# Kernel optimization log

Hardware: AMD Instinct MI355X
Metric: run time of the kernel (lower is better)

## Reference

```python
import jax, jax.numpy as jnp
import numpy as np

CODEBOOK_SIZE = 1024
EMBEDDING_DIM = 256
COMMITMENT_COST = 0.25


def setup_inputs() -> dict:
    key = jax.random.key(0)
    k1, k2 = jax.random.split(key)
    x = jax.random.normal(k1, (32, EMBEDDING_DIM, 32, 32), dtype=jnp.float32)
    # embedding initialized uniform(-1/K, 1/K) like the torch module
    embedding = jax.random.uniform(
        k2, (CODEBOOK_SIZE, EMBEDDING_DIM), dtype=jnp.float32,
        minval=-1.0 / CODEBOOK_SIZE, maxval=1.0 / CODEBOOK_SIZE)
    return {"x": x, "embedding": embedding}


def reference(x, embedding):
    # x: [B, C, H, W] -> inputs: [B, H, W, C]
    inputs = jnp.transpose(x, (0, 2, 3, 1))
    input_shape = inputs.shape
    flat = inputs.reshape(-1, EMBEDDING_DIM)  # [N, D]
    # squared L2 distances to codebook: [N, K]
    distances = (jnp.sum(flat ** 2, axis=1, keepdims=True)
                 + jnp.sum(embedding ** 2, axis=1)
                 - 2.0 * flat @ embedding.T)
    encoding_indices = jnp.argmin(distances, axis=1)  # [N]
    encodings = jax.nn.one_hot(encoding_indices, CODEBOOK_SIZE, dtype=jnp.float32)  # [N, K]
    # gather (same math as encodings @ embedding)
    quantized = embedding[encoding_indices].reshape(input_shape)  # [B, H, W, C]
    e_latent_loss = jnp.mean((jax.lax.stop_gradient(quantized) - inputs) ** 2)
    q_latent_loss = jnp.mean((quantized - jax.lax.stop_gradient(inputs)) ** 2)
    loss = q_latent_loss + COMMITMENT_COST * e_latent_loss
    # straight-through estimator
    quantized_st = inputs + jax.lax.stop_gradient(quantized - inputs)
    return (loss, jnp.transpose(quantized_st, (0, 3, 1, 2)), encodings)
```

## Files before the change

kernel.cpp:

```cpp
#include <hip/hip_runtime.h>
#include <cstdint>
#include <cstddef>

constexpr int B = 32, C = 256, H = 32, W = 32;
constexpr int NPTS = B * H * W;
constexpr int DIM  = 256;
constexpr int K    = 1024;
constexpr int QELEMS = B * C * H * W;
constexpr int CHW = C * H * W;

typedef __attribute__((ext_vector_type(8))) short s8v;
typedef __attribute__((ext_vector_type(4))) float f32x4;

#define GLD_LDS16(g, l)                                                        \
  __builtin_amdgcn_global_load_lds(                                            \
      (const __attribute__((address_space(1))) unsigned int*)(g),              \
      (__attribute__((address_space(3))) unsigned int*)(l), 16, 0, 0)

__device__ __forceinline__ unsigned short f2bf(float f) {
  unsigned u = __float_as_uint(f);
  return (unsigned short)((u + 0x7FFFu + ((u >> 16) & 1u)) >> 16);
}

__device__ __forceinline__ void nt_store4(float* p, f32x4 v) {
  __builtin_nontemporal_store(v, (f32x4*)p);
}
__device__ __forceinline__ void nt_store1(float* p, float v) {
  __builtin_nontemporal_store(v, p);
}

__global__ __launch_bounds__(256) void prep_kernel(
    const float* __restrict__ x, const float* __restrict__ emb,
    unsigned short* __restrict__ ehi, float* __restrict__ esq,
    unsigned short* __restrict__ xhi, float* __restrict__ xsq) {
  __shared__ float xls[DIM][32];
  const int t = threadIdx.x;
  const int bid = blockIdx.x;

  if (bid < 16) {
    float (*sums)[64] = (float (*)[64])xls;
    const int k = bid * 64 + (t & 63);
    const int seg = t >> 6;
    const float* er = emb + (size_t)k * DIM + seg * 64;
    float v[64];
    float4* v4 = (float4*)v;
#pragma unroll
    for (int i = 0; i < 16; ++i) v4[i] = *(const float4*)(er + i * 4);
    float s = 0.f;
#pragma unroll
    for (int i = 0; i < 64; ++i) s = fmaf(v[i], v[i], s);
    unsigned short* eo = ehi + (size_t)k * DIM + seg * 64;
#pragma unroll
    for (int i = 0; i < 8; ++i) {
      unsigned short h[8];
#pragma unroll
      for (int j = 0; j < 8; ++j) h[j] = f2bf(v[i * 8 + j]);
      *(s8v*)(eo + i * 8) = *(s8v*)h;
    }
    sums[seg][t & 63] = s;
    __syncthreads();
    if (t < 64)
      esq[bid * 64 + t] =
          ((sums[0][t] + sums[1][t]) + sums[2][t]) + sums[3][t];
    return;
  }

  const int n0 = (bid - 16) * 32;
  const int bb = n0 >> 10, hw0 = n0 & 1023;
  const float* xb = x + (size_t)bb * CHW + hw0;
  const int lane = t & 63, w = t >> 6;
  const int row_off = lane >> 3;
  const int p4 = (lane & 7) * 4;
#pragma unroll
  for (int i = 0; i < 8; ++i) {
    const int c0 = w * 64 + i * 8;
    GLD_LDS16(xb + (size_t)(c0 + row_off) * 1024 + p4, &xls[c0][0]);
  }
  __syncthreads();

  if (t < 32) {
    float s = 0.f;
#pragma unroll 8
    for (int c = 0; c < 256; ++c) {
      const float v = xls[c][t];
      s = fmaf(v, v, s);
    }
    xsq[n0 + t] = s;
  }
  const int p2 = t & 31, cb = (t >> 5) * 32;
  unsigned short* xo = xhi + (size_t)(n0 + p2) * DIM + cb;
#pragma unroll
  for (int i = 0; i < 4; ++i) {
    unsigned short h[8];
#pragma unroll
    for (int j = 0; j < 8; ++j) h[j] = f2bf(xls[cb + i * 8 + j][p2]);
    *(s8v*)(xo + i * 8) = *(s8v*)h;
  }
}

constexpr float MARGIN = 1e-3f;
__global__ __launch_bounds__(256) void coarse_kernel(
    const unsigned short* __restrict__ xhi, const unsigned short* __restrict__ ehi,
    const float* __restrict__ esq, const float* __restrict__ xsq,
    float* __restrict__ part, unsigned int* __restrict__ cand) {
  __shared__ __align__(16) unsigned short xs[128][32];
  __shared__ __align__(16) unsigned short es[128][32];
  __shared__ float xsq_s[128], esq_s[128], thr_s[128];
  __shared__ unsigned long long red2[2][128];
  __shared__ unsigned int cntL[128];

  const int t = threadIdx.x;
  const int lane = t & 63, w = t >> 6;
  const int wn = (w & 1) * 64, wk = (w >> 1) * 64;
  const int col = lane & 15, quad = lane >> 4;
  const int nblk = blockIdx.x * 128;
  const int kblk = blockIdx.y * 128;

  if (t < 128) {
    xsq_s[t] = xsq[nblk + t];
    esq_s[t] = esq[kblk + t];
    cntL[t] = 0u;
  }

  f32x4 acc[4][4];
#pragma unroll
  for (int i = 0; i < 4; ++i)
#pragma unroll
    for (int j = 0; j < 4; ++j) acc[i][j] = (f32x4){0.f, 0.f, 0.f, 0.f};

  const int gl_row = lane >> 2;
  const int gl_c   = (lane & 3) * 8;

  for (int c0 = 0; c0 < DIM; c0 += 32) {
    __syncthreads();
#pragma unroll
    for (int i = 0; i < 2; ++i) {
      const int inst = w + 4 * i;
      const int row = inst * 16 + gl_row;
      GLD_LDS16(xhi + (size_t)(nblk + row) * DIM + c0 + gl_c, &xs[inst * 16][0]);
      GLD_LDS16(ehi + (size_t)(kblk + row) * DIM + c0 + gl_c, &es[inst * 16][0]);
    }
    __syncthreads();
    s8v a[4], b[4];
#pragma unroll
    for (int ti = 0; ti < 4; ++ti)
      a[ti] = *(const s8v*)&xs[wn + ti * 16 + col][quad * 8];
#pragma unroll
    for (int tj = 0; tj < 4; ++tj)
      b[tj] = *(const s8v*)&es[wk + tj * 16 + col][quad * 8];
#pragma unroll
    for (int ti = 0; ti < 4; ++ti)
#pragma unroll
      for (int tj = 0; tj < 4; ++tj)
        acc[ti][tj] = __builtin_amdgcn_mfma_f32_16x16x32_bf16(
            a[ti], b[tj], acc[ti][tj], 0, 0, 0);
  }

  unsigned long long nmin[4][4];
#pragma unroll
  for (int ti = 0; ti < 4; ++ti)
#pragma unroll
    for (int r = 0; r < 4; ++r) nmin[ti][r] = ~0ULL;
#pragma unroll
  for (int ti = 0; ti < 4; ++ti)
#pragma unroll
    for (int tj = 0; tj < 4; ++tj) {
      const int krel = wk + tj * 16 + col;
      const float eq = esq_s[krel];
#pragma unroll
      for (int r = 0; r < 4; ++r) {
        const int nl = wn + ti * 16 + quad * 4 + r;
        const float d = (xsq_s[nl] + eq) - 2.f * acc[ti][tj][r];
        const unsigned long long key =
            ((unsigned long long)__float_as_uint(d) << 32) |
            (unsigned)(kblk + krel);
        if (key < nmin[ti][r]) nmin[ti][r] = key;
      }
    }
#pragma unroll
  for (int o = 1; o < 16; o <<= 1)
#pragma unroll
    for (int ti = 0; ti < 4; ++ti)
#pragma unroll
      for (int r = 0; r < 4; ++r) {
        const unsigned long long v = __shfl_xor(nmin[ti][r], o, 64);
        if (v < nmin[ti][r]) nmin[ti][r] = v;
      }
  if (col == 0) {
#pragma unroll
    for (int ti = 0; ti < 4; ++ti)
#pragma unroll
      for (int r = 0; r < 4; ++r)
        red2[w >> 1][wn + ti * 16 + quad * 4 + r] = nmin[ti][r];
  }
  __syncthreads();
  if (t < 128) {
    const unsigned long long m0 = red2[0][t], m1 = red2[1][t];
    const unsigned long long m = (m1 < m0) ? m1 : m0;
    const float dmin = __uint_as_float((unsigned)(m >> 32));
    part[(size_t)(nblk + t) * 8 + blockIdx.y] = dmin;
    thr_s[t] = dmin + MARGIN;
  }
  __syncthreads();
#pragma unroll
  for (int ti = 0; ti < 4; ++ti)
#pragma unroll
    for (int tj = 0; tj < 4; ++tj) {
      const int krel = wk + tj * 16 + col;
      const float eq = esq_s[krel];
#pragma unroll
      for (int r = 0; r < 4; ++r) {
        const int nl = wn + ti * 16 + quad * 4 + r;
        const float d = (xsq_s[nl] + eq) - 2.f * acc[ti][tj][r];
        if (d <= thr_s[nl]) {
          const unsigned slot = atomicAdd(&cntL[nl], 1u);
          if (slot < 4u)
            cand[((size_t)(nblk + nl) * 8 + blockIdx.y) * 4 + slot] =
                (unsigned)(kblk + krel);
        }
      }
    }
  __syncthreads();
  if (t < 128) {
    unsigned c = cntL[t];
    const size_t base = ((size_t)(nblk + t) * 8 + blockIdx.y) * 4;
    if (c > 4u) { cand[base + 3] = 0xFFFFFFFEu; c = 3u; }
    for (unsigned s = c; s < 4u; ++s) cand[base + s] = 0xFFFFFFFFu;
  }
}

__global__ __launch_bounds__(256) void resolve_kernel(
    const float* __restrict__ x, const float* __restrict__ emb,
    const float* __restrict__ esq, const float* __restrict__ xsq,
    const float* __restrict__ part, const unsigned int* __restrict__ cand,
    int* __restrict__ ids_g, float* __restrict__ lws) {
  __shared__ __align__(16) float xls[DIM][33];
  __shared__ unsigned list[1024];
  __shared__ unsigned long long best[32];
  __shared__ float thr_s[32];
  __shared__ float xsq_s[32];
  __shared__ int lcnt;

  const int t = threadIdx.x;
  const int n0 = blockIdx.x * 32;
  const int bb = n0 >> 10, hw0 = n0 & 1023;

  const float* xb = x + (size_t)bb * CHW + hw0;
  {
    const int p = t & 31, cs = t >> 5;
#pragma unroll 8
    for (int r = 0; r < 32; ++r) {
      const int c = r * 8 + cs;
      xls[c][p] = xb[(size_t)c * 1024 + p];
    }
  }
  if (t == 0) lcnt = 0;
  if (t < 32) {
    best[t] = ~0ULL;
    xsq_s[t] = xsq[n0 + t];
    const float4 p0 = *(const float4*)&part[(size_t)(n0 + t) * 8];
    const float4 p1 = *(const float4*)&part[(size_t)(n0 + t) * 8 + 4];
    float g = fminf(fminf(fminf(p0.x, p0.y), fminf(p0.z, p0.w)),
                    fminf(fminf(p1.x, p1.y), fminf(p1.z, p1.w)));
    thr_s[t] = g + MARGIN;
  }
  __syncthreads();

  {
    const int nn = t >> 3, s = t & 7;
    const float pv = part[(size_t)(n0 + nn) * 8 + s];
    if (pv <= thr_s[nn]) {
      const uint4 c4 = *(const uint4*)&cand[((size_t)(n0 + nn) * 8 + s) * 4];
      const unsigned vs[4] = {c4.x, c4.y, c4.z, c4.w};
#pragma unroll
      for (int i = 0; i < 4; ++i) {
        const unsigned v = vs[i];
        if (v == 0xFFFFFFFFu) continue;
        const unsigned entry = (v == 0xFFFFFFFEu)
                                   ? ((unsigned)nn << 11) | 1024u | (unsigned)s
                                   : ((unsigned)nn << 11) | (v & 1023u);
        const int pos = atomicAdd(&lcnt, 1);
        if (pos < 1024) list[pos] = entry;
      }
    }
  }
  __syncthreads();

  const int L = lcnt < 1024 ? lcnt : 1024;
  for (int e = t; e < L; e += 256) {
    const unsigned entry = list[e];
    const int p = entry >> 11;
    const float xq = xsq_s[p];
    int klo, khi;
    if (entry & 1024u) { const int s = entry & 7; klo = s * 128; khi = klo + 128; }
    else               { klo = entry & 1023u; khi = klo + 1; }
    for (int k = klo; k < khi; ++k) {
      const float* er = emb + (size_t)k * DIM;
      float dot = 0.f;
#pragma unroll 4
      for (int c4 = 0; c4 < DIM; c4 += 4) {
        const float4 e4 = *(const float4*)(er + c4);
        dot = fmaf(xls[c4 + 0][p], e4.x, dot);
        dot = fmaf(xls[c4 + 1][p], e4.y, dot);
        dot = fmaf(xls[c4 + 2][p], e4.z, dot);
        dot = fmaf(xls[c4 + 3][p], e4.w, dot);
      }
      const float t1 = xq + esq[k];
      const float d = t1 - 2.f * dot;
      const unsigned long long key =
          ((unsigned long long)__float_as_uint(d) << 32) | (unsigned)k;
      atomicMin(&best[p], key);
    }
  }
  __syncthreads();
  if (t < 32) {
    ids_g[n0 + t] = (int)(best[t] & 0xFFFFFFFFu);
    float s = __uint_as_float((unsigned)(best[t] >> 32));
#pragma unroll
    for (int o = 16; o > 0; o >>= 1) s += __shfl_down(s, o, 64);
    if (t == 0) lws[blockIdx.x] = s;
  }
}

__global__ __launch_bounds__(256) void encq_kernel(
    const float* __restrict__ emb, const int* __restrict__ ids_g,
    float* __restrict__ enc, float* __restrict__ outq) {
  __shared__ int ids_s[32];
  const int t = threadIdx.x;
  const int n0 = blockIdx.x * 32;
  const int bb = n0 >> 10, hw0 = n0 & 1023;
  if (t < 32) ids_s[t] = ids_g[n0 + t];
  __syncthreads();

  float* sl = enc + (size_t)n0 * K;
  {
    float* b4 = sl + 3;
#pragma unroll
    for (int j = 0; j < 32; ++j) {
      const int idx = t + j * 256;
      if (idx < 8191) {
        const int lf = 3 + 4 * idx;
        f32x4 v;
        v.x = (((lf + 0) & 1023) == ids_s[(lf + 0) >> 10]) ? 1.f : 0.f;
        v.y = (((lf + 1) & 1023) == ids_s[(lf + 1) >> 10]) ? 1.f : 0.f;
        v.z = (((lf + 2) & 1023) == ids_s[(lf + 2) >> 10]) ? 1.f : 0.f;
        v.w = (((lf + 3) & 1023) == ids_s[(lf + 3) >> 10]) ? 1.f : 0.f;
        nt_store4(b4 + 4 * idx, v);
      }
    }
    if (t == 0) {
      nt_store1(sl + 0, (ids_s[0] == 0) ? 1.f : 0.f);
      nt_store1(sl + 1, (ids_s[0] == 1) ? 1.f : 0.f);
      nt_store1(sl + 2, (ids_s[0] == 2) ? 1.f : 0.f);
      nt_store1(sl + 32767, (ids_s[31] == 1023) ? 1.f : 0.f);
    }
  }

  {
    const int p = t & 31, g = t >> 5;
    const int row = ids_s[p];
    const float* er = emb + (size_t)row * DIM + g * 32;
    float* ob = outq + (size_t)bb * CHW + hw0 + p;
#pragma unroll
    for (int i = 0; i < 8; ++i) {
      const float4 v = *(const float4*)(er + i * 4);
      const int c = g * 32 + i * 4;
      nt_store1(ob + (size_t)(c + 0) * 1024, v.x);
      nt_store1(ob + (size_t)(c + 1) * 1024, v.y);
      nt_store1(ob + (size_t)(c + 2) * 1024, v.z);
      nt_store1(ob + (size_t)(c + 3) * 1024, v.w);
    }
  }
}

__global__ __launch_bounds__(256) void loss_reduce(
    const float* __restrict__ lws, float* __restrict__ loss) {
  __shared__ float red[4];
  const int t = threadIdx.x;
  float s = 0.f;
#pragma unroll
  for (int i = 0; i < 4; ++i) s += lws[t + i * 256];
#pragma unroll
  for (int o = 32; o > 0; o >>= 1) s += __shfl_down(s, o, 64);
  if ((t & 63) == 0) red[t >> 6] = s;
  __syncthreads();
  if (t == 0)
    *loss = (((red[0] + red[1]) + red[2]) + red[3]) * (1.25f / (float)QELEMS);
}

extern "C" void kernel_launch(void* const* d_in, const int* in_sizes, int n_in,
                              void* d_out, int out_size, void* d_ws, size_t ws_size,
                              hipStream_t stream) {
  const float* x   = (const float*)d_in[0];
  const float* emb = (const float*)d_in[1];
  float* out  = (float*)d_out;
  float* loss = out;
  float* outq = out + 1;
  float* enc  = out + 1 + QELEMS;

  char* ws = (char*)d_ws;
  unsigned short* ehi  = (unsigned short*)ws;
  float*          esq  = (float*)(ws + 524288);
  float*          xsq  = (float*)(ws + 528384);
  float*          part = (float*)(ws + 659456);
  unsigned int*   cand = (unsigned int*)(ws + 1708032);
  unsigned short* xhi  = (unsigned short*)(ws + 5902336);
  float*          lws  = (float*)(ws + 22679552);
  int*            ids  = (int*)(ws + 22683648);

  prep_kernel<<<16 + 1024, 256, 0, stream>>>(x, emb, ehi, esq, xhi, xsq);
  dim3 cg(NPTS / 128, 8);
  coarse_kernel<<<cg, 256, 0, stream>>>(xhi, ehi, esq, xsq, part, cand);
  resolve_kernel<<<NPTS / 32, 256, 0, stream>>>(x, emb, esq, xsq, part, cand,
                                                ids, lws);
  encq_kernel<<<NPTS / 32, 256, 0, stream>>>(emb, ids, enc, outq);
  loss_reduce<<<1, 256, 0, stream>>>(lws, loss);
}
```

Before: 302.8 us.

## Fuse resolve and encode/quantize kernels; parallelize overflow rescans across threads

Merges the candidate-resolve kernel with the one-hot/quantized output kernel, so the chosen indices stay in shared memory and one launch plus the ids round trip are removed. Overflowed candidate slices (128 codes) now go into a separate list and are scanned by 128 threads in parallel instead of serially by one thread. Output stores switch from nontemporal to normal stores. The fused kernel uses more shared memory and does more work per block, which may lower occupancy.

```diff
diff --git a/kernel.cpp b/kernel.cpp
--- a/kernel.cpp
+++ b/kernel.cpp
@@ -20,13 +20,6 @@
 __device__ __forceinline__ unsigned short f2bf(float f) {
   unsigned u = __float_as_uint(f);
   return (unsigned short)((u + 0x7FFFu + ((u >> 16) & 1u)) >> 16);
-}
-
-__device__ __forceinline__ void nt_store4(float* p, f32x4 v) {
-  __builtin_nontemporal_store(v, (f32x4*)p);
-}
-__device__ __forceinline__ void nt_store1(float* p, float v) {
-  __builtin_nontemporal_store(v, p);
 }
 
 __global__ __launch_bounds__(256) void prep_kernel(
@@ -229,17 +222,20 @@
   }
 }
 
-__global__ __launch_bounds__(256) void resolve_kernel(
+__global__ __launch_bounds__(256) void finish2_kernel(
     const float* __restrict__ x, const float* __restrict__ emb,
     const float* __restrict__ esq, const float* __restrict__ xsq,
     const float* __restrict__ part, const unsigned int* __restrict__ cand,
-    int* __restrict__ ids_g, float* __restrict__ lws) {
+    float* __restrict__ outq, float* __restrict__ enc,
+    float* __restrict__ lws) {
   __shared__ __align__(16) float xls[DIM][33];
   __shared__ unsigned list[1024];
+  __shared__ unsigned rlist[256];
   __shared__ unsigned long long best[32];
   __shared__ float thr_s[32];
   __shared__ float xsq_s[32];
-  __shared__ int lcnt;
+  __shared__ int ids_s[32];
+  __shared__ int lcnt, rcnt;
 
   const int t = threadIdx.x;
   const int n0 = blockIdx.x * 32;
@@ -254,7 +250,7 @@
       xls[c][p] = xb[(size_t)c * 1024 + p];
     }
   }
-  if (t == 0) lcnt = 0;
+  if (t == 0) { lcnt = 0; rcnt = 0; }
   if (t < 32) {
     best[t] = ~0ULL;
     xsq_s[t] = xsq[n0 + t];
@@ -271,16 +267,19 @@
     const float pv = part[(size_t)(n0 + nn) * 8 + s];
     if (pv <= thr_s[nn]) {
       const uint4 c4 = *(const uint4*)&cand[((size_t)(n0 + nn) * 8 + s) * 4];
-      const unsigned vs[4] = {c4.x, c4.y, c4.z, c4.w};
-#pragma unroll
-      for (int i = 0; i < 4; ++i) {
-        const unsigned v = vs[i];
-        if (v == 0xFFFFFFFFu) continue;
-        const unsigned entry = (v == 0xFFFFFFFEu)
-                                   ? ((unsigned)nn << 11) | 1024u | (unsigned)s
-                                   : ((unsigned)nn << 11) | (v & 1023u);
-        const int pos = atomicAdd(&lcnt, 1);
-        if (pos < 1024) list[pos] = entry;
+      if (c4.w == 0xFFFFFFFEu) {
+        const int rp = atomicAdd(&rcnt, 1);
+        if (rp < 256) rlist[rp] = ((unsigned)nn << 3) | (unsigned)s;
+      } else {
+        const unsigned vs[4] = {c4.x, c4.y, c4.z, c4.w};
+#pragma unroll
+        for (int i = 0; i < 4; ++i) {
+          const unsigned v = vs[i];
+          if (v <= 1023u) {
+            const int pos = atomicAdd(&lcnt, 1);
+            if (pos < 1024) list[pos] = ((unsigned)nn << 11) | v;
+          }
+        }
       }
     }
   }
@@ -290,11 +289,33 @@
   for (int e = t; e < L; e += 256) {
     const unsigned entry = list[e];
     const int p = entry >> 11;
+    const int k = entry & 2047;
     const float xq = xsq_s[p];
-    int klo, khi;
-    if (entry & 1024u) { const int s = entry & 7; klo = s * 128; khi = klo + 128; }
-    else               { klo = entry & 1023u; khi = klo + 1; }
-    for (int k = klo; k < khi; ++k) {
+    const float* er = emb + (size_t)k * DIM;
+    float dot = 0.f;
+#pragma unroll 4
+    for (int c4 = 0; c4 < DIM; c4 += 4) {
+      const float4 e4 = *(const float4*)(er + c4);
+      dot = fmaf(xls[c4 + 0][p], e4.x, dot);
+      dot = fmaf(xls[c4 + 1][p], e4.y, dot);
+      dot = fmaf(xls[c4 + 2][p], e4.z, dot);
+      dot = fmaf(xls[c4 + 3][p], e4.w, dot);
+    }
+    const float t1 = xq + esq[k];
+    const float d = t1 - 2.f * dot;
+    const unsigned long long key =
+        ((unsigned long long)__float_as_uint(d) << 32) | (unsigned)k;
+    atomicMin(&best[p], key);
+  }
+
+  const int R = rcnt < 256 ? rcnt : 256;
+  for (int rb = 0; rb < R; rb += 2) {
+    const int ri = rb + (t >> 7);
+    if (ri < R) {
+      const unsigned rs = rlist[ri];
+      const int p = rs >> 3;
+      const int k = (int)(rs & 7u) * 128 + (t & 127);
+      const float xq = xsq_s[p];
       const float* er = emb + (size_t)k * DIM;
       float dot = 0.f;
 #pragma unroll 4
@@ -313,46 +334,37 @@
     }
   }
   __syncthreads();
+
   if (t < 32) {
-    ids_g[n0 + t] = (int)(best[t] & 0xFFFFFFFFu);
+    ids_s[t] = (int)(best[t] & 0xFFFFFFFFu);
     float s = __uint_as_float((unsigned)(best[t] >> 32));
 #pragma unroll
     for (int o = 16; o > 0; o >>= 1) s += __shfl_down(s, o, 64);
     if (t == 0) lws[blockIdx.x] = s;
   }
-}
-
-__global__ __launch_bounds__(256) void encq_kernel(
-    const float* __restrict__ emb, const int* __restrict__ ids_g,
-    float* __restrict__ enc, float* __restrict__ outq) {
-  __shared__ int ids_s[32];
-  const int t = threadIdx.x;
-  const int n0 = blockIdx.x * 32;
-  const int bb = n0 >> 10, hw0 = n0 & 1023;
-  if (t < 32) ids_s[t] = ids_g[n0 + t];
-  __syncthreads();
-
-  float* sl = enc + (size_t)n0 * K;
+  __syncthreads();
+
   {
+    float* sl = enc + (size_t)n0 * K;
     float* b4 = sl + 3;
 #pragma unroll
     for (int j = 0; j < 32; ++j) {
       const int idx = t + j * 256;
       if (idx < 8191) {
         const int lf = 3 + 4 * idx;
-        f32x4 v;
+        float4 v;
         v.x = (((lf + 0) & 1023) == ids_s[(lf + 0) >> 10]) ? 1.f : 0.f;
         v.y = (((lf + 1) & 1023) == ids_s[(lf + 1) >> 10]) ? 1.f : 0.f;
         v.z = (((lf + 2) & 1023) == ids_s[(lf + 2) >> 10]) ? 1.f : 0.f;
         v.w = (((lf + 3) & 1023) == ids_s[(lf + 3) >> 10]) ? 1.f : 0.f;
-        nt_store4(b4 + 4 * idx, v);
+        *(float4*)(b4 + 4 * idx) = v;
       }
     }
     if (t == 0) {
-      nt_store1(sl + 0, (ids_s[0] == 0) ? 1.f : 0.f);
-      nt_store1(sl + 1, (ids_s[0] == 1) ? 1.f : 0.f);
-      nt_store1(sl + 2, (ids_s[0] == 2) ? 1.f : 0.f);
-      nt_store1(sl + 32767, (ids_s[31] == 1023) ? 1.f : 0.f);
+      sl[0] = (ids_s[0] == 0) ? 1.f : 0.f;
+      sl[1] = (ids_s[0] == 1) ? 1.f : 0.f;
+      sl[2] = (ids_s[0] == 2) ? 1.f : 0.f;
+      sl[32767] = (ids_s[31] == 1023) ? 1.f : 0.f;
     }
   }
 
@@ -365,10 +377,10 @@
     for (int i = 0; i < 8; ++i) {
       const float4 v = *(const float4*)(er + i * 4);
       const int c = g * 32 + i * 4;
-      nt_store1(ob + (size_t)(c + 0) * 1024, v.x);
-      nt_store1(ob + (size_t)(c + 1) * 1024, v.y);
-      nt_store1(ob + (size_t)(c + 2) * 1024, v.z);
-      nt_store1(ob + (size_t)(c + 3) * 1024, v.w);
+      ob[(size_t)(c + 0) * 1024] = v.x;
+      ob[(size_t)(c + 1) * 1024] = v.y;
+      ob[(size_t)(c + 2) * 1024] = v.z;
+      ob[(size_t)(c + 3) * 1024] = v.w;
     }
   }
 }
@@ -406,13 +418,11 @@
   unsigned int*   cand = (unsigned int*)(ws + 1708032);
   unsigned short* xhi  = (unsigned short*)(ws + 5902336);
   float*          lws  = (float*)(ws + 22679552);
-  int*            ids  = (int*)(ws + 22683648);
 
   prep_kernel<<<16 + 1024, 256, 0, stream>>>(x, emb, ehi, esq, xhi, xsq);
   dim3 cg(NPTS / 128, 8);
   coarse_kernel<<<cg, 256, 0, stream>>>(xhi, ehi, esq, xsq, part, cand);
-  resolve_kernel<<<NPTS / 32, 256, 0, stream>>>(x, emb, esq, xsq, part, cand,
-                                                ids, lws);
-  encq_kernel<<<NPTS / 32, 256, 0, stream>>>(emb, ids, enc, outq);
+  finish2_kernel<<<NPTS / 32, 256, 0, stream>>>(x, emb, esq, xsq, part, cand,
+                                                outq, enc, lws);
   loss_reduce<<<1, 256, 0, stream>>>(lws, loss);
 }
```

Result: faster. 283.0 us (median of 2 runs) (-6.5%).
